# Optimization experiments

Hardware: AMD Instinct MI355X
Metric: run time of the kernel (lower is better)

## Reference

```python
import jax, jax.numpy as jnp
import numpy as np

DEPTH = 8
LEAVES = 2 ** DEPTH            # 256 leaf values
N_NODES = 2 ** DEPTH - 1       # 255 internal split nodes
TEMP = 1.0
EPS_P = 1e-5
EPS_V = 1e-10
EPS_MASK = 1e-12


def setup_inputs() -> dict:
    key = jax.random.key(0)
    k1, k2, k3 = jax.random.split(key, 3)
    B, D, O = 8192, 512, 64
    x = jax.random.normal(k1, (B, D), dtype=jnp.float32)
    # BaseSplitter assumed: single linear layer + temperature sigmoid
    Ws = jax.random.normal(k2, (D, N_NODES), dtype=jnp.float32) * (1.0 / np.sqrt(D))
    bs = jnp.zeros((N_NODES,), dtype=jnp.float32)
    # xavier_uniform_ init for leaf value table (LEAVES, O)
    limit = float(np.sqrt(6.0 / (LEAVES + O)))
    value = jax.random.uniform(k3, (LEAVES, O), dtype=jnp.float32, minval=-limit, maxval=limit)
    return {"x": x, "Ws": Ws, "bs": bs, "value": value}


def _sdt_forward(x, Ws, bs, value):
    B = x.shape[0]
    leaves = value.shape[0]
    # splitter: per-node routing probabilities, shape (B, 2^depth - 1)
    probs = jax.nn.sigmoid((x @ Ws + bs) / TEMP)

    accum = jnp.zeros((B, leaves), dtype=jnp.float32)
    reg = jnp.float32(0.0)
    for d in range(DEPTH):  # small fixed loop over tree depth
        s, e = 2 ** d - 1, 2 ** (d + 1) - 1
        p = probs[:, s:e]                     # (B, 2^d) nodes at depth d
        logp = jnp.log(jnp.clip(p, EPS_P))
        log1mp = jnp.log(jnp.clip(1.0 - p, EPS_P))
        # regularization: sum over nodes of mean over batch
        reg = reg + (-0.5) * (2.0 ** (-d)) * jnp.log(jnp.clip(p * (1.0 - p), EPS_P)).mean(axis=0).sum()
        # interleave [logp_i, log1mp_i] per node, then broadcast each entry
        # over its span of leaves/2^(d+1) leaf slots
        contrib = jnp.stack([logp, log1mp], axis=-1).reshape(B, 2 ** (d + 1))
        rep = leaves // (2 ** (d + 1))
        accum = accum + jnp.broadcast_to(contrib[:, :, None], (B, 2 ** (d + 1), rep)).reshape(B, leaves)

    sign = jnp.sign(value)                                    # (L, O)
    logval = jnp.log(jnp.clip(jnp.abs(value), EPS_V))          # (L, O)
    ret = logval[None, :, :] + accum[:, :, None]               # (B, L, O)
    log_pos = jax.nn.logsumexp(ret + jnp.log((sign > 0).astype(jnp.float32) + EPS_MASK), axis=1)
    log_neg = jax.nn.logsumexp(ret + jnp.log((sign < 0).astype(jnp.float32) + EPS_MASK), axis=1)
    out = jnp.exp(log_pos) - jnp.exp(log_neg)                  # (B, O)
    return out, reg


def reference(x, Ws, bs, value):
    return _sdt_forward(x, Ws, bs, value)
```

## Files before the change

kernel.cpp:

```cpp
#include <hip/hip_runtime.h>


typedef __attribute__((ext_vector_type(8))) _Float16 half8;
typedef __attribute__((ext_vector_type(4))) _Float16 half4;
typedef __attribute__((ext_vector_type(4))) float floatx4;

constexpr int O = 64;
constexpr int XSTR = 520;
constexpr int PSTR = 280;
constexpr int LSTR = 260;

__global__ __launch_bounds__(256) void sdt_pre(
    const float* __restrict__ Ws, const float* __restrict__ value,
    _Float16* __restrict__ wt, _Float16* __restrict__ vt,
    float* __restrict__ reg_slot)
{
  const int bid = blockIdx.x, t = threadIdx.x;
  if (bid < 64) {
    const int k0 = bid * 8;
    const int n = t;
    const int T = n >> 4, r = n & 15;
    const int c = k0 >> 5, q = (k0 >> 3) & 3;
    _Float16 v8[8];
#pragma unroll
    for (int kk = 0; kk < 8; ++kk) {
      float f = (n < 255) ? Ws[(size_t)(k0 + kk) * 255 + n] : 0.f;
      v8[kk] = (_Float16)f;
    }
    *(half8*)&wt[(size_t)(T * 16 + c) * 512 + (q * 16 + r) * 8] = *(half8*)v8;
  } else {
    const int k0 = (bid - 64) * 64;
#pragma unroll
    for (int j = 0; j < 16; ++j) {
      int e = t + j * 256;
      int k = k0 + (e >> 6), n = e & 63;
      float f = value[(size_t)k * O + n];
      int T = n >> 4, r = n & 15, kc = k >> 5, q = (k >> 3) & 3, jj = k & 7;
      vt[(size_t)(T * 8 + kc) * 512 + (q * 16 + r) * 8 + jj] = (_Float16)f;
    }
    if (bid == 64 && t == 0) *reg_slot = 0.f;
  }
}

__global__ __launch_bounds__(512, 2) void sdt_main(
    const float* __restrict__ x, const _Float16* __restrict__ wt,
    const _Float16* __restrict__ vt, const float* __restrict__ bs,
    float* __restrict__ out, float* __restrict__ reg_out)
{
  __shared__ __align__(16) char smem[33280 + 17920];
  _Float16* xh_s = (_Float16*)smem;
  float*    L_s  = (float*)smem;
  _Float16* P_h  = (_Float16*)(smem + 33280);
  __shared__ float red_s[8];

  const int t = threadIdx.x, lane = t & 63, w = t >> 6;
  const int q = lane >> 4, r16 = lane & 15;
  const int R0 = blockIdx.x * 32;

  {
    const int row = t >> 4, l4 = (t & 15) * 4;
    const float* xrow = x + (size_t)(R0 + row) * 512;
#pragma unroll
    for (int i = 0; i < 8; ++i) {
      const int k = l4 + i * 64;
      float4 v = *(const float4*)(xrow + k);
      half4 h = {(_Float16)v.x, (_Float16)v.y, (_Float16)v.z, (_Float16)v.w};
      *(half4*)&xh_s[row * XSTR + k] = h;
    }
  }
  __syncthreads();

  const _Float16* pb0 = wt + (size_t)(2 * w) * 16 * 512 + lane * 8;
  const _Float16* pb1 = wt + (size_t)(2 * w + 1) * 16 * 512 + lane * 8;
  const int a0off = r16 * XSTR, a1off = (16 + r16) * XSTR;

  floatx4 acc00 = {0,0,0,0}, acc01 = {0,0,0,0}, acc10 = {0,0,0,0}, acc11 = {0,0,0,0};
  half8 B0 = *(const half8*)pb0, B1 = *(const half8*)pb1;

#pragma unroll
  for (int c = 0; c < 16; ++c) {
    half8 n0, n1;
    if (c < 15) {
      n0 = *(const half8*)(pb0 + (c + 1) * 512);
      n1 = *(const half8*)(pb1 + (c + 1) * 512);
    }
    half8 a0 = *(const half8*)&xh_s[a0off + c * 32 + q * 8];
    half8 a1 = *(const half8*)&xh_s[a1off + c * 32 + q * 8];
    acc00 = __builtin_amdgcn_mfma_f32_16x16x32_f16(a0, B0, acc00, 0, 0, 0);
    acc01 = __builtin_amdgcn_mfma_f32_16x16x32_f16(a0, B1, acc01, 0, 0, 0);
    acc10 = __builtin_amdgcn_mfma_f32_16x16x32_f16(a1, B0, acc10, 0, 0, 0);
    acc11 = __builtin_amdgcn_mfma_f32_16x16x32_f16(a1, B1, acc11, 0, 0, 0);
    if (c < 15) { B0 = n0; B1 = n1; }
  }
  __syncthreads();

  {
    const int c0 = w * 32 + r16, c1 = c0 + 16;
#pragma unroll
    for (int r = 0; r < 4; ++r) {
      int row0 = q * 4 + r, row1 = row0 + 16;
      L_s[row0 * LSTR + c0] = acc00[r];
      L_s[row0 * LSTR + c1] = acc01[r];
      L_s[row1 * LSTR + c0] = acc10[r];
      L_s[row1 * LSTR + c1] = acc11[r];
    }
  }
  __syncthreads();

  {
    const int col = t & 255, half = t >> 8;
    float rsum = 0.f;
    if (col < 255) {
      float b = bs[col];
      for (int r = half * 16; r < half * 16 + 16; ++r) {
        float z = L_s[r * LSTR + col] + b;
        float p = 1.f / (1.f + __expf(-z));
        L_s[r * LSTR + col] = p;
        rsum += __logf(fmaxf(p * (1.f - p), 1e-5f));
      }
      int dd = 31 - __clz(col + 1);
      rsum *= -0.5f / (8192.0f * (float)(1 << dd));
    }
#pragma unroll
    for (int off = 32; off; off >>= 1) rsum += __shfl_down(rsum, off, 64);
    if (lane == 0) red_s[w] = rsum;
  }
  __syncthreads();
  if (t == 0) {
    float s = 0.f;
#pragma unroll
    for (int i = 0; i < 8; ++i) s += red_s[i];
    atomicAdd(reg_out, s);
  }

  {
    const int g8 = t & 31, rp = t >> 5;
    const int Lb = g8 * 8;
#pragma unroll
    for (int rr = 0; rr < 2; ++rr) {
      const int row = rp * 2 + rr;
      const float* Lr = &L_s[row * LSTR];
      float pre = 1.f;
#pragma unroll
      for (int dd = 0; dd < 5; ++dd) {
        float p = Lr[(1 << dd) - 1 + (Lb >> (8 - dd))];
        float br = ((Lb >> (7 - dd)) & 1) ? (1.f - p) : p;
        pre *= fmaxf(br, 1e-5f);
      }
      float p5 = Lr[31 + g8];
      float s5a = fmaxf(p5, 1e-5f), s5b = fmaxf(1.f - p5, 1e-5f);
      float p6a = Lr[63 + 2 * g8], p6b = Lr[63 + 2 * g8 + 1];
      float p7v[4];
#pragma unroll
      for (int m = 0; m < 4; ++m) p7v[m] = Lr[127 + 4 * g8 + m];
      _Float16 ph[8];
#pragma unroll
      for (int j = 0; j < 8; ++j) {
        float s5 = (j & 4) ? s5b : s5a;
        float p6 = (j & 4) ? p6b : p6a;
        float s6 = fmaxf((j & 2) ? (1.f - p6) : p6, 1e-5f);
        float p7 = p7v[j >> 1];
        float s7 = fmaxf((j & 1) ? (1.f - p7) : p7, 1e-5f);
        ph[j] = (_Float16)(pre * s5 * s6 * s7);
      }
      *(half8*)&P_h[row * PSTR + Lb] = *(half8*)ph;
    }
  }
  __syncthreads();

  {
    const int tm = w & 1, tn = w >> 1;
    floatx4 C = {0, 0, 0, 0};
    const _Float16* vb = vt + (size_t)(tn * 8) * 512 + lane * 8;
    const _Float16* pa = &P_h[(tm * 16 + r16) * PSTR + q * 8];
#pragma unroll
    for (int kc = 0; kc < 8; ++kc) {
      half8 A8 = *(const half8*)(pa + kc * 32);
      half8 B8 = *(const half8*)(vb + kc * 512);
      C = __builtin_amdgcn_mfma_f32_16x16x32_f16(A8, B8, C, 0, 0, 0);
    }
    const int col = tn * 16 + r16;
#pragma unroll
    for (int r = 0; r < 4; ++r) {
      int row = tm * 16 + q * 4 + r;
      out[(size_t)(R0 + row) * O + col] = C[r];
    }
  }
}

extern "C" void kernel_launch(void* const* d_in, const int* in_sizes, int n_in,
                              void* d_out, int out_size, void* d_ws, size_t ws_size,
                              hipStream_t stream) {
  const float* x     = (const float*)d_in[0];
  const float* Ws    = (const float*)d_in[1];
  const float* bs    = (const float*)d_in[2];
  const float* value = (const float*)d_in[3];
  float* outp = (float*)d_out;
  float* reg_slot = outp + (size_t)8192 * O;
  _Float16* wt = (_Float16*)d_ws;
  _Float16* vt = wt + 256 * 512;

  sdt_pre<<<68, 256, 0, stream>>>(Ws, value, wt, vt, reg_slot);
  sdt_main<<<256, 512, 0, stream>>>(x, wt, vt, bs, outp, reg_slot);
}
```

Before: 84.35 us.

## Halve rows per block and widen preprocessing grid to fill more CUs

The main kernel now handles 16 rows per block with 256 threads, down from 32 rows with 512 threads. Each wave computes four 16-column tiles of the splitter GEMM from one shared A fragment, and the grid doubles to 512 blocks. The preprocessing kernel is split across 160 blocks instead of 68 so each block does less serial work. This spreads work over more of the device's compute units. In exchange each B fragment loaded from global memory is reused across fewer rows, so weight traffic per output row roughly doubles.

After: 87.22 us. 1.03x slower.

```diff
diff --git a/kernel.cpp b/kernel.cpp
--- a/kernel.cpp
+++ b/kernel.cpp
@@ -16,46 +16,46 @@
     float* __restrict__ reg_slot)
 {
   const int bid = blockIdx.x, t = threadIdx.x;
-  if (bid < 64) {
-    const int k0 = bid * 8;
+  if (bid < 128) {
+    const int k0 = bid * 4;
     const int n = t;
     const int T = n >> 4, r = n & 15;
-    const int c = k0 >> 5, q = (k0 >> 3) & 3;
-    _Float16 v8[8];
-#pragma unroll
-    for (int kk = 0; kk < 8; ++kk) {
+    const int c = k0 >> 5, q = (k0 >> 3) & 3, j0 = k0 & 7;
+    _Float16 v4[4];
+#pragma unroll
+    for (int kk = 0; kk < 4; ++kk) {
       float f = (n < 255) ? Ws[(size_t)(k0 + kk) * 255 + n] : 0.f;
-      v8[kk] = (_Float16)f;
-    }
-    *(half8*)&wt[(size_t)(T * 16 + c) * 512 + (q * 16 + r) * 8] = *(half8*)v8;
+      v4[kk] = (_Float16)f;
+    }
+    *(half4*)&wt[(size_t)(T * 16 + c) * 512 + (q * 16 + r) * 8 + j0] = *(half4*)v4;
   } else {
-    const int k0 = (bid - 64) * 64;
-#pragma unroll
-    for (int j = 0; j < 16; ++j) {
-      int e = t + j * 256;
-      int k = k0 + (e >> 6), n = e & 63;
+    const int e0 = (bid - 128) * 512 + t;
+#pragma unroll
+    for (int j = 0; j < 2; ++j) {
+      int e = e0 + j * 256;
+      int k = e >> 6, n = e & 63;
       float f = value[(size_t)k * O + n];
       int T = n >> 4, r = n & 15, kc = k >> 5, q = (k >> 3) & 3, jj = k & 7;
       vt[(size_t)(T * 8 + kc) * 512 + (q * 16 + r) * 8 + jj] = (_Float16)f;
     }
-    if (bid == 64 && t == 0) *reg_slot = 0.f;
+    if (bid == 128 && t == 0) *reg_slot = 0.f;
   }
 }
 
-__global__ __launch_bounds__(512, 2) void sdt_main(
+__global__ __launch_bounds__(256, 2) void sdt_main(
     const float* __restrict__ x, const _Float16* __restrict__ wt,
     const _Float16* __restrict__ vt, const float* __restrict__ bs,
     float* __restrict__ out, float* __restrict__ reg_out)
 {
-  __shared__ __align__(16) char smem[33280 + 17920];
+  __shared__ __align__(16) char smem[16640 + 8960];
   _Float16* xh_s = (_Float16*)smem;
   float*    L_s  = (float*)smem;
-  _Float16* P_h  = (_Float16*)(smem + 33280);
-  __shared__ float red_s[8];
+  _Float16* P_h  = (_Float16*)(smem + 16640);
+  __shared__ float red_s[4];
 
   const int t = threadIdx.x, lane = t & 63, w = t >> 6;
   const int q = lane >> 4, r16 = lane & 15;
-  const int R0 = blockIdx.x * 32;
+  const int R0 = blockIdx.x * 16;
 
   {
     const int row = t >> 4, l4 = (t & 15) * 4;
@@ -70,49 +70,53 @@
   }
   __syncthreads();
 
-  const _Float16* pb0 = wt + (size_t)(2 * w) * 16 * 512 + lane * 8;
-  const _Float16* pb1 = wt + (size_t)(2 * w + 1) * 16 * 512 + lane * 8;
-  const int a0off = r16 * XSTR, a1off = (16 + r16) * XSTR;
-
-  floatx4 acc00 = {0,0,0,0}, acc01 = {0,0,0,0}, acc10 = {0,0,0,0}, acc11 = {0,0,0,0};
+  const _Float16* pb0 = wt + (size_t)(w * 4 + 0) * 16 * 512 + lane * 8;
+  const _Float16* pb1 = wt + (size_t)(w * 4 + 1) * 16 * 512 + lane * 8;
+  const _Float16* pb2 = wt + (size_t)(w * 4 + 2) * 16 * 512 + lane * 8;
+  const _Float16* pb3 = wt + (size_t)(w * 4 + 3) * 16 * 512 + lane * 8;
+  const int a0off = r16 * XSTR + q * 8;
+
+  floatx4 acc0 = {0,0,0,0}, acc1 = {0,0,0,0}, acc2 = {0,0,0,0}, acc3 = {0,0,0,0};
   half8 B0 = *(const half8*)pb0, B1 = *(const half8*)pb1;
+  half8 B2 = *(const half8*)pb2, B3 = *(const half8*)pb3;
 
 #pragma unroll
   for (int c = 0; c < 16; ++c) {
-    half8 n0, n1;
+    half8 n0, n1, n2, n3;
     if (c < 15) {
       n0 = *(const half8*)(pb0 + (c + 1) * 512);
       n1 = *(const half8*)(pb1 + (c + 1) * 512);
-    }
-    half8 a0 = *(const half8*)&xh_s[a0off + c * 32 + q * 8];
-    half8 a1 = *(const half8*)&xh_s[a1off + c * 32 + q * 8];
-    acc00 = __builtin_amdgcn_mfma_f32_16x16x32_f16(a0, B0, acc00, 0, 0, 0);
-    acc01 = __builtin_amdgcn_mfma_f32_16x16x32_f16(a0, B1, acc01, 0, 0, 0);
-    acc10 = __builtin_amdgcn_mfma_f32_16x16x32_f16(a1, B0, acc10, 0, 0, 0);
-    acc11 = __builtin_amdgcn_mfma_f32_16x16x32_f16(a1, B1, acc11, 0, 0, 0);
-    if (c < 15) { B0 = n0; B1 = n1; }
-  }
-  __syncthreads();
-
-  {
-    const int c0 = w * 32 + r16, c1 = c0 + 16;
-#pragma unroll
-    for (int r = 0; r < 4; ++r) {
-      int row0 = q * 4 + r, row1 = row0 + 16;
-      L_s[row0 * LSTR + c0] = acc00[r];
-      L_s[row0 * LSTR + c1] = acc01[r];
-      L_s[row1 * LSTR + c0] = acc10[r];
-      L_s[row1 * LSTR + c1] = acc11[r];
-    }
-  }
-  __syncthreads();
-
-  {
-    const int col = t & 255, half = t >> 8;
+      n2 = *(const half8*)(pb2 + (c + 1) * 512);
+      n3 = *(const half8*)(pb3 + (c + 1) * 512);
+    }
+    half8 a = *(const half8*)&xh_s[a0off + c * 32];
+    acc0 = __builtin_amdgcn_mfma_f32_16x16x32_f16(a, B0, acc0, 0, 0, 0);
+    acc1 = __builtin_amdgcn_mfma_f32_16x16x32_f16(a, B1, acc1, 0, 0, 0);
+    acc2 = __builtin_amdgcn_mfma_f32_16x16x32_f16(a, B2, acc2, 0, 0, 0);
+    acc3 = __builtin_amdgcn_mfma_f32_16x16x32_f16(a, B3, acc3, 0, 0, 0);
+    if (c < 15) { B0 = n0; B1 = n1; B2 = n2; B3 = n3; }
+  }
+  __syncthreads();
+
+  {
+#pragma unroll
+    for (int i = 0; i < 4; ++i) {
+      const floatx4& A = (i == 0) ? acc0 : (i == 1) ? acc1 : (i == 2) ? acc2 : acc3;
+      const int c0 = (w * 4 + i) * 16 + r16;
+#pragma unroll
+      for (int r = 0; r < 4; ++r)
+        L_s[(q * 4 + r) * LSTR + c0] = A[r];
+    }
+  }
+  __syncthreads();
+
+  {
+    const int col = t;
     float rsum = 0.f;
     if (col < 255) {
       float b = bs[col];
-      for (int r = half * 16; r < half * 16 + 16; ++r) {
+#pragma unroll 4
+      for (int r = 0; r < 16; ++r) {
         float z = L_s[r * LSTR + col] + b;
         float p = 1.f / (1.f + __expf(-z));
         L_s[r * LSTR + col] = p;
@@ -126,12 +130,8 @@
     if (lane == 0) red_s[w] = rsum;
   }
   __syncthreads();
-  if (t == 0) {
-    float s = 0.f;
-#pragma unroll
-    for (int i = 0; i < 8; ++i) s += red_s[i];
-    atomicAdd(reg_out, s);
-  }
+  if (t == 0)
+    atomicAdd(reg_out, red_s[0] + red_s[1] + red_s[2] + red_s[3]);
 
   {
     const int g8 = t & 31, rp = t >> 5;
@@ -169,22 +169,19 @@
   __syncthreads();
 
   {
-    const int tm = w & 1, tn = w >> 1;
     floatx4 C = {0, 0, 0, 0};
-    const _Float16* vb = vt + (size_t)(tn * 8) * 512 + lane * 8;
-    const _Float16* pa = &P_h[(tm * 16 + r16) * PSTR + q * 8];
+    const _Float16* vb = vt + (size_t)(w * 8) * 512 + lane * 8;
+    const _Float16* pa = &P_h[r16 * PSTR + q * 8];
 #pragma unroll
     for (int kc = 0; kc < 8; ++kc) {
       half8 A8 = *(const half8*)(pa + kc * 32);
       half8 B8 = *(const half8*)(vb + kc * 512);
       C = __builtin_amdgcn_mfma_f32_16x16x32_f16(A8, B8, C, 0, 0, 0);
     }
-    const int col = tn * 16 + r16;
-#pragma unroll
-    for (int r = 0; r < 4; ++r) {
-      int row = tm * 16 + q * 4 + r;
-      out[(size_t)(R0 + row) * O + col] = C[r];
-    }
+    const int col = w * 16 + r16;
+#pragma unroll
+    for (int r = 0; r < 4; ++r)
+      out[(size_t)(R0 + q * 4 + r) * O + col] = C[r];
   }
 }
 
@@ -200,6 +197,6 @@
   _Float16* wt = (_Float16*)d_ws;
   _Float16* vt = wt + 256 * 512;
 
-  sdt_pre<<<68, 256, 0, stream>>>(Ws, value, wt, vt, reg_slot);
-  sdt_main<<<256, 512, 0, stream>>>(x, wt, vt, bs, outp, reg_slot);
+  sdt_pre<<<160, 256, 0, stream>>>(Ws, value, wt, vt, reg_slot);
+  sdt_main<<<512, 256, 0, stream>>>(x, wt, vt, bs, outp, reg_slot);
 }
```
